# Optimization experiments

Measured on AMD Instinct MI355X. Metric: run time of the kernel, lower is better.

## Reference

```python
import jax, jax.numpy as jnp
import numpy as np

N, E = 50000, 800000          # nodes, edges (before self-loops)
IN, HID, HEADS, OUT = 128, 32, 4, 128
NEG_SLOPE = 0.2               # PyG GATv2Conv default negative_slope


def setup_inputs() -> dict:
    key = jax.random.key(0)
    ks = jax.random.split(key, 16)
    s = 0.05
    f32 = jnp.float32
    return {
        "x": jax.random.normal(ks[0], (N, IN), f32),
        "edge_index": jax.random.randint(ks[1], (2, E), 0, N, jnp.int32),
        # layer 1: in=128 -> heads=4, out=32 (concat)
        "W1l": jax.random.normal(ks[2], (IN, HEADS * HID), f32) * s,
        "b1l": jnp.zeros((HEADS * HID,), f32),
        "W1r": jax.random.normal(ks[3], (IN, HEADS * HID), f32) * s,
        "b1r": jnp.zeros((HEADS * HID,), f32),
        "att1": jax.random.normal(ks[4], (HEADS, HID), f32) * s,
        "bias1": jnp.zeros((HEADS * HID,), f32),
        # layer 2: in=128 -> heads=1, out=128 (mean/no-concat)
        "W2l": jax.random.normal(ks[5], (HEADS * HID, OUT), f32) * s,
        "b2l": jnp.zeros((OUT,), f32),
        "W2r": jax.random.normal(ks[6], (HEADS * HID, OUT), f32) * s,
        "b2r": jnp.zeros((OUT,), f32),
        "att2": jax.random.normal(ks[7], (1, OUT), f32) * s,
        "bias2": jnp.zeros((OUT,), f32),
    }


def _gatv2_conv(x, src, dst, Wl, bl, Wr, br, att, bias, concat):
    """PyG GATv2Conv (share_weights=False), self-loops already in (src, dst)."""
    n = x.shape[0]
    heads, c = att.shape
    xl = (x @ Wl + bl).reshape(n, heads, c)   # source-side transform
    xr = (x @ Wr + br).reshape(n, heads, c)   # target-side transform
    h = jax.nn.leaky_relu(xl[src] + xr[dst], NEG_SLOPE)      # [E, H, C]
    logits = jnp.einsum('ehc,hc->eh', h, att)                # [E, H]
    # segment softmax over incoming edges of each dst node (self-loops make every segment nonempty)
    m = jax.ops.segment_max(logits, dst, num_segments=n)     # [N, H]
    p = jnp.exp(logits - m[dst])
    denom = jax.ops.segment_sum(p, dst, num_segments=n)
    alpha = p / denom[dst]                                   # [E, H]
    out = jax.ops.segment_sum(xl[src] * alpha[:, :, None], dst, num_segments=n)  # [N, H, C]
    out = out.reshape(n, heads * c) if concat else out.mean(axis=1)
    return out + bias


def reference(x, edge_index, W1l, b1l, W1r, b1r, att1, bias1,
              W2l, b2l, W2r, b2r, att2, bias2):
    n = x.shape[0]
    loops = jnp.arange(n, dtype=edge_index.dtype)            # add_self_loops=True
    src = jnp.concatenate([edge_index[0], loops])
    dst = jnp.concatenate([edge_index[1], loops])
    h = jax.nn.elu(_gatv2_conv(x, src, dst, W1l, b1l, W1r, b1r, att1, bias1, True))
    # dropout is identity in eval mode
    return _gatv2_conv(h, src, dst, W2l, b2l, W2r, b2r, att2, bias2, False)
```

## Files before the change

kernel.cpp:

```cpp
#include <hip/hip_runtime.h>
#include <hip/hip_bf16.h>
#include <cstdint>


typedef __attribute__((ext_vector_type(8))) short  bf16x8;
typedef __attribute__((ext_vector_type(4))) float  f32x4;

__device__ inline uint16_t f2bf(float x) {
    union { __hip_bfloat16 b; uint16_t u; } cv;
    cv.b = __float2bfloat16(x);
    return cv.u;
}

__global__ __launch_bounds__(256) void f32_to_bf16(const float* __restrict__ in,
                                                   uint16_t* __restrict__ outp, int n4)
{
    int i = blockIdx.x * blockDim.x + threadIdx.x;
    if (i < n4) {
        float4 v = reinterpret_cast<const float4*>(in)[i];
        ushort4 o = { f2bf(v.x), f2bf(v.y), f2bf(v.z), f2bf(v.w) };
        reinterpret_cast<ushort4*>(outp)[i] = o;
    }
}

__global__ __launch_bounds__(256) void w_to_bf16T(const float* __restrict__ W,
                                                  uint16_t* __restrict__ WT)
{
    int i = blockIdx.x * blockDim.x + threadIdx.x;
    if (i < 128 * 128) {
        int k = i >> 7, c = i & 127;
        WT[c * 128 + k] = f2bf(W[i]);
    }
}

template <bool OUT_BF16>
__global__ __launch_bounds__(256) void gemm_mfma(
    const uint16_t* __restrict__ A, const uint16_t* __restrict__ WT,
    const float* __restrict__ bias, void* __restrict__ Y, int M)
{
    __shared__ uint16_t WT_lds[64][136];
    const int col0 = blockIdx.y * 64;
    const int row0 = blockIdx.x * 128;
    const int tid  = threadIdx.x;
    const int w    = tid >> 6, l = tid & 63;
    const int cl   = l & 15;
    const int kb   = (l >> 4) * 8;

    for (int i = tid; i < 64 * 16; i += 256) {
        const int c = i >> 4, ch = i & 15;
        const uint4 v = *reinterpret_cast<const uint4*>(&WT[(size_t)(col0 + c) * 128 + ch * 8]);
        *reinterpret_cast<uint4*>(&WT_lds[c][ch * 8]) = v;
    }
    __syncthreads();

    const int mrow = row0 + w * 32 + cl;
    const int rA0 = mrow < M ? mrow : M - 1;
    const int rA1 = (mrow + 16) < M ? (mrow + 16) : M - 1;
    const uint16_t* a0p = A + (size_t)rA0 * 128 + kb;
    const uint16_t* a1p = A + (size_t)rA1 * 128 + kb;

    f32x4 acc[2][4] = {};
#pragma unroll
    for (int ks = 0; ks < 4; ++ks) {
        const bf16x8 a0 = *reinterpret_cast<const bf16x8*>(a0p + ks * 32);
        const bf16x8 a1 = *reinterpret_cast<const bf16x8*>(a1p + ks * 32);
#pragma unroll
        for (int n = 0; n < 4; ++n) {
            const bf16x8 b = *reinterpret_cast<const bf16x8*>(&WT_lds[n * 16 + cl][ks * 32 + kb]);
            acc[0][n] = __builtin_amdgcn_mfma_f32_16x16x32_bf16(a0, b, acc[0][n], 0, 0, 0);
            acc[1][n] = __builtin_amdgcn_mfma_f32_16x16x32_bf16(a1, b, acc[1][n], 0, 0, 0);
        }
    }

    const int rbase = row0 + w * 32 + (l >> 4) * 4;
#pragma unroll
    for (int m = 0; m < 2; ++m) {
#pragma unroll
        for (int n = 0; n < 4; ++n) {
            const int col = col0 + n * 16 + cl;
            const float bv = bias[col];
#pragma unroll
            for (int j = 0; j < 4; ++j) {
                const int row = rbase + m * 16 + j;
                if (row < M) {
                    const float v = acc[m][n][j] + bv;
                    if constexpr (OUT_BF16)
                        ((uint16_t*)Y)[(size_t)row * 128 + col] = f2bf(v);
                    else
                        ((float*)Y)[(size_t)row * 128 + col] = v;
                }
            }
        }
    }
}

__global__ __launch_bounds__(256) void hist_kernel(const int* __restrict__ dst, int E,
                                                   int* __restrict__ count)
{
    for (int i = blockIdx.x * blockDim.x + threadIdx.x; i < E;
         i += gridDim.x * blockDim.x)
        atomicAdd(&count[dst[i]], 1);
}

__global__ __launch_bounds__(1024) void scan_offsets(const int* __restrict__ count,
                                                     int* __restrict__ offset,
                                                     int* __restrict__ cursor, int N)
{
    __shared__ int wsum[16];
    __shared__ int carry_s;
    const int tid = threadIdx.x;
    const int lane = tid & 63, w = tid >> 6;
    if (tid == 0) carry_s = 0;
    __syncthreads();
    for (int base = 0; base < N; base += 1024) {
        int i = base + tid;
        int v = (i < N) ? (count[i] + 1) : 0;
        int x = v;
#pragma unroll
        for (int off = 1; off < 64; off <<= 1) {
            int y = __shfl_up(x, off);
            if (lane >= off) x += y;
        }
        if (lane == 63) wsum[w] = x;
        __syncthreads();
        if (tid < 16) {
            int s2 = wsum[tid];
#pragma unroll
            for (int off = 1; off < 16; off <<= 1) {
                int y = __shfl_up(s2, off);
                if (tid >= off) s2 += y;
            }
            wsum[tid] = s2;
        }
        __syncthreads();
        int carry = carry_s;
        int inc = x + ((w > 0) ? wsum[w - 1] : 0) + carry;
        if (i < N) { offset[i] = inc - v; cursor[i] = inc - v; }
        __syncthreads();
        if (tid == 1023) carry_s = inc;
        __syncthreads();
    }
    if (tid == 0) offset[N] = carry_s;
}

__global__ __launch_bounds__(256) void scatter_kernel(const int* __restrict__ src,
                                                      const int* __restrict__ dst, int E,
                                                      int* __restrict__ cursor,
                                                      int* __restrict__ srcids)
{
    for (int i = blockIdx.x * blockDim.x + threadIdx.x; i < E;
         i += gridDim.x * blockDim.x) {
        int p = atomicAdd(&cursor[dst[i]], 1);
        srcids[p] = src[i];
    }
}

__global__ __launch_bounds__(256) void selfloop_kernel(int* __restrict__ cursor,
                                                       int* __restrict__ srcids, int N)
{
    int i = blockIdx.x * blockDim.x + threadIdx.x;
    if (i < N) {
        int p = atomicAdd(&cursor[i], 1);
        srcids[p] = i;
    }
}

template <int HEADS, bool ELU, bool OUT_BF16>
__global__ __launch_bounds__(256) void gat_aggregate(
    const uint32_t* __restrict__ xl2,
    const float* __restrict__ xr,
    const int* __restrict__ offset, const int* __restrict__ srcids,
    const float* __restrict__ att, const float* __restrict__ bias,
    void* __restrict__ out, int N)
{
    const int wid  = (blockIdx.x * blockDim.x + threadIdx.x) >> 6;
    const int lane = threadIdx.x & 63;
    if (wid >= N) return;

    const int f0 = lane * 2;
    const float2 rr = *reinterpret_cast<const float2*>(&xr[(size_t)wid * 128 + f0]);
    const float av0 = att[f0], av1 = att[f0 + 1];

    float acc0 = 0.0f, acc1 = 0.0f, d = 0.0f;
    const int beg = offset[wid], end = offset[wid + 1];

    int i = beg;
    for (; i + 2 <= end; i += 2) {
        const int sA = srcids[i];
        const int sB = srcids[i + 1];
        const uint32_t vA = xl2[(size_t)sA * 64 + lane];
        const uint32_t vB = xl2[(size_t)sB * 64 + lane];
        const float aA0 = __uint_as_float(vA << 16);
        const float aA1 = __uint_as_float(vA & 0xFFFF0000u);
        const float aB0 = __uint_as_float(vB << 16);
        const float aB1 = __uint_as_float(vB & 0xFFFF0000u);
        float tA0 = aA0 + rr.x, tA1 = aA1 + rr.y;
        float tB0 = aB0 + rr.x, tB1 = aB1 + rr.y;
        tA0 = tA0 > 0.0f ? tA0 : 0.2f * tA0;
        tA1 = tA1 > 0.0f ? tA1 : 0.2f * tA1;
        tB0 = tB0 > 0.0f ? tB0 : 0.2f * tB0;
        tB1 = tB1 > 0.0f ? tB1 : 0.2f * tB1;
        float wA = tA0 * av0 + tA1 * av1;
        float wB = tB0 * av0 + tB1 * av1;
        if (HEADS == 4) {
#pragma unroll
            for (int off = 1; off < 16; off <<= 1) {
                wA += __shfl_xor(wA, off);
                wB += __shfl_xor(wB, off);
            }
        } else {
#pragma unroll
            for (int off = 1; off < 64; off <<= 1) {
                wA += __shfl_xor(wA, off);
                wB += __shfl_xor(wB, off);
            }
        }
        const float pA = __expf(wA);
        const float pB = __expf(wB);
        acc0 += aA0 * pA; acc1 += aA1 * pA; d += pA;
        acc0 += aB0 * pB; acc1 += aB1 * pB; d += pB;
    }
    if (i < end) {
        const int s = srcids[i];
        const uint32_t v = xl2[(size_t)s * 64 + lane];
        const float a0 = __uint_as_float(v << 16);
        const float a1 = __uint_as_float(v & 0xFFFF0000u);
        float t0 = a0 + rr.x, t1 = a1 + rr.y;
        t0 = t0 > 0.0f ? t0 : 0.2f * t0;
        t1 = t1 > 0.0f ? t1 : 0.2f * t1;
        float w = t0 * av0 + t1 * av1;
        if (HEADS == 4) {
#pragma unroll
            for (int off = 1; off < 16; off <<= 1) w += __shfl_xor(w, off);
        } else {
#pragma unroll
            for (int off = 1; off < 64; off <<= 1) w += __shfl_xor(w, off);
        }
        const float p = __expf(w);
        acc0 += a0 * p; acc1 += a1 * p; d += p;
    }

    float v0 = acc0 / d + bias[f0];
    float v1 = acc1 / d + bias[f0 + 1];
    if (ELU) {
        v0 = v0 > 0.0f ? v0 : expm1f(v0);
        v1 = v1 > 0.0f ? v1 : expm1f(v1);
    }
    if constexpr (OUT_BF16) {
        const uint32_t pk = (uint32_t)f2bf(v0) | ((uint32_t)f2bf(v1) << 16);
        ((uint32_t*)out)[(size_t)wid * 64 + lane] = pk;
    } else {
        float2 o = { v0, v1 };
        *reinterpret_cast<float2*>(&((float*)out)[(size_t)wid * 128 + f0]) = o;
    }
}

extern "C" void kernel_launch(void* const* d_in, const int* in_sizes, int n_in,
                              void* d_out, int out_size, void* d_ws, size_t ws_size,
                              hipStream_t stream)
{
    const float* x     = (const float*)d_in[0];
    const int*   ei    = (const int*)  d_in[1];
    const float* W1l   = (const float*)d_in[2];
    const float* b1l   = (const float*)d_in[3];
    const float* W1r   = (const float*)d_in[4];
    const float* b1r   = (const float*)d_in[5];
    const float* att1  = (const float*)d_in[6];
    const float* bias1 = (const float*)d_in[7];
    const float* W2l   = (const float*)d_in[8];
    const float* b2l   = (const float*)d_in[9];
    const float* W2r   = (const float*)d_in[10];
    const float* b2r   = (const float*)d_in[11];
    const float* att2  = (const float*)d_in[12];
    const float* bias2 = (const float*)d_in[13];
    float* out = (float*)d_out;

    const int N    = in_sizes[0] / 128;
    const int E    = in_sizes[1] / 2;
    const int Etot = E + N;
    const int* srcp = ei;
    const int* dstp = ei + E;

    int* count  = (int*)d_ws;
    int* offset = count + N;
    int* cursor = offset + N + 1;
    int* srcids = cursor + N;
    size_t int_elems = (size_t)3 * N + 1 + Etot;
    int_elems = (int_elems + 3) & ~(size_t)3;
    uint32_t* base32 = (uint32_t*)d_ws + int_elems;
    uint16_t* x_bf   = (uint16_t*)base32;
    uint16_t* wt1l   = x_bf + (size_t)N * 128;
    uint16_t* wt1r   = wt1l + 128 * 128;
    uint16_t* wt2l   = wt1r + 128 * 128;
    uint16_t* wt2r   = wt2l + 128 * 128;
    float*    xr     = (float*)(wt2r + 128 * 128);
    uint16_t* h_bf   = (uint16_t*)(xr + (size_t)N * 128);
    uint16_t* xl_bf  = h_bf + (size_t)N * 128;
    uint32_t* h2  = (uint32_t*)h_bf;
    uint32_t* xl2 = (uint32_t*)xl_bf;

    f32_to_bf16<<<(N * 32 + 255) / 256, 256, 0, stream>>>(x, x_bf, N * 32);
    w_to_bf16T<<<64, 256, 0, stream>>>(W1l, wt1l);
    w_to_bf16T<<<64, 256, 0, stream>>>(W1r, wt1r);
    w_to_bf16T<<<64, 256, 0, stream>>>(W2l, wt2l);
    w_to_bf16T<<<64, 256, 0, stream>>>(W2r, wt2r);

    hipMemsetAsync(count, 0, (size_t)N * sizeof(int), stream);
    hist_kernel<<<2048, 256, 0, stream>>>(dstp, E, count);
    scan_offsets<<<1, 1024, 0, stream>>>(count, offset, cursor, N);
    scatter_kernel<<<2048, 256, 0, stream>>>(srcp, dstp, E, cursor, srcids);
    selfloop_kernel<<<(N + 255) / 256, 256, 0, stream>>>(cursor, srcids, N);

    dim3 gG((N + 127) / 128, 2);
    const int ablocks = (N + 3) / 4;

    gemm_mfma<true ><<<gG, 256, 0, stream>>>(x_bf, wt1l, b1l, xl_bf, N);
    gemm_mfma<false><<<gG, 256, 0, stream>>>(x_bf, wt1r, b1r, xr,    N);
    gat_aggregate<4, true, true><<<ablocks, 256, 0, stream>>>(
        xl2, xr, offset, srcids, att1, bias1, h_bf, N);
    gemm_mfma<true ><<<gG, 256, 0, stream>>>(h_bf, wt2l, b2l, xl_bf, N);
    gemm_mfma<false><<<gG, 256, 0, stream>>>(h_bf, wt2r, b2r, xr,    N);
    gat_aggregate<1, false, false><<<ablocks, 256, 0, stream>>>(
        xl2, xr, offset, srcids, att2, bias2, out, N);
}
```

Before: 448.2 us.

## Parallelize offset scan, merge weight and self-loop kernels, unroll aggregation by four

Replaces the single-block serial scan over all nodes with a three-kernel multi-block scan (block sums, 64-entry mid scan, apply). It also merges the four weight transpose launches into one and folds the self-loop insertion into the scatter kernel. The edge loop in the aggregation kernel now processes four neighbours per iteration to put more gathers in flight. These changes target the latency of the serial scan and launch overhead, at the cost of extra registers in the aggregation and an assumption that the number of scan blocks is at most 64.

Result: faster. 384.0 us (-14.3%).

```diff
diff --git a/kernel.cpp b/kernel.cpp
--- a/kernel.cpp
+++ b/kernel.cpp
@@ -23,14 +23,18 @@
     }
 }
 
-__global__ __launch_bounds__(256) void w_to_bf16T(const float* __restrict__ W,
-                                                  uint16_t* __restrict__ WT)
+__global__ __launch_bounds__(256) void w4_to_bf16T(
+    const float* __restrict__ W0, const float* __restrict__ W1,
+    const float* __restrict__ W2, const float* __restrict__ W3,
+    uint16_t* __restrict__ T0, uint16_t* __restrict__ T1,
+    uint16_t* __restrict__ T2, uint16_t* __restrict__ T3)
 {
     int i = blockIdx.x * blockDim.x + threadIdx.x;
-    if (i < 128 * 128) {
-        int k = i >> 7, c = i & 127;
-        WT[c * 128 + k] = f2bf(W[i]);
-    }
+    const int which = i >> 14, j = i & 16383;
+    const int k = j >> 7, c = j & 127;
+    const float* W = which == 0 ? W0 : which == 1 ? W1 : which == 2 ? W2 : W3;
+    uint16_t*   T = which == 0 ? T0 : which == 1 ? T1 : which == 2 ? T2 : T3;
+    T[c * 128 + k] = f2bf(W[j]);
 }
 
 template <bool OUT_BF16>
@@ -102,66 +106,94 @@
         atomicAdd(&count[dst[i]], 1);
 }
 
-__global__ __launch_bounds__(1024) void scan_offsets(const int* __restrict__ count,
-                                                     int* __restrict__ offset,
-                                                     int* __restrict__ cursor, int N)
-{
-    __shared__ int wsum[16];
-    __shared__ int carry_s;
+__global__ __launch_bounds__(256) void scan_blocksums(const int* __restrict__ count,
+                                                      int* __restrict__ bsum, int N)
+{
+    __shared__ int wsum[4];
+    const int tid = threadIdx.x, lane = tid & 63, w = tid >> 6;
+    const int base = blockIdx.x * 1024 + tid * 4;
+    int s = 0;
+#pragma unroll
+    for (int j = 0; j < 4; ++j) {
+        int idx = base + j;
+        s += (idx < N) ? (count[idx] + 1) : 0;
+    }
+#pragma unroll
+    for (int off = 1; off < 64; off <<= 1) s += __shfl_xor(s, off);
+    if (lane == 0) wsum[w] = s;
+    __syncthreads();
+    if (tid == 0) bsum[blockIdx.x] = wsum[0] + wsum[1] + wsum[2] + wsum[3];
+}
+
+__global__ __launch_bounds__(64) void scan_mid(const int* __restrict__ bsum,
+                                               int* __restrict__ bpre,
+                                               int* __restrict__ offset, int nb, int N)
+{
     const int tid = threadIdx.x;
-    const int lane = tid & 63, w = tid >> 6;
-    if (tid == 0) carry_s = 0;
+    int v = (tid < nb) ? bsum[tid] : 0;
+    int x = v;
+#pragma unroll
+    for (int off = 1; off < 64; off <<= 1) {
+        int y = __shfl_up(x, off);
+        if (tid >= off) x += y;
+    }
+    if (tid < nb) bpre[tid] = x - v;
+    const int total = __shfl(x, 63);
+    if (tid == 0) offset[N] = total;
+}
+
+__global__ __launch_bounds__(256) void scan_apply(const int* __restrict__ count,
+                                                  const int* __restrict__ bpre,
+                                                  int* __restrict__ offset,
+                                                  int* __restrict__ cursor, int N)
+{
+    __shared__ int wsum[4];
+    const int tid = threadIdx.x, lane = tid & 63, w = tid >> 6;
+    const int base = blockIdx.x * 1024 + tid * 4;
+    int v[4];
+    int s = 0;
+#pragma unroll
+    for (int j = 0; j < 4; ++j) {
+        int idx = base + j;
+        v[j] = (idx < N) ? (count[idx] + 1) : 0;
+        s += v[j];
+    }
+    int x = s;
+#pragma unroll
+    for (int off = 1; off < 64; off <<= 1) {
+        int y = __shfl_up(x, off);
+        if (lane >= off) x += y;
+    }
+    if (lane == 63) wsum[w] = x;
     __syncthreads();
-    for (int base = 0; base < N; base += 1024) {
-        int i = base + tid;
-        int v = (i < N) ? (count[i] + 1) : 0;
-        int x = v;
-#pragma unroll
-        for (int off = 1; off < 64; off <<= 1) {
-            int y = __shfl_up(x, off);
-            if (lane >= off) x += y;
-        }
-        if (lane == 63) wsum[w] = x;
-        __syncthreads();
-        if (tid < 16) {
-            int s2 = wsum[tid];
-#pragma unroll
-            for (int off = 1; off < 16; off <<= 1) {
-                int y = __shfl_up(s2, off);
-                if (tid >= off) s2 += y;
-            }
-            wsum[tid] = s2;
-        }
-        __syncthreads();
-        int carry = carry_s;
-        int inc = x + ((w > 0) ? wsum[w - 1] : 0) + carry;
-        if (i < N) { offset[i] = inc - v; cursor[i] = inc - v; }
-        __syncthreads();
-        if (tid == 1023) carry_s = inc;
-        __syncthreads();
-    }
-    if (tid == 0) offset[N] = carry_s;
+    int wpre = 0;
+#pragma unroll
+    for (int k = 0; k < 4; ++k) wpre += (k < w) ? wsum[k] : 0;
+    int run = bpre[blockIdx.x] + wpre + (x - s);
+#pragma unroll
+    for (int j = 0; j < 4; ++j) {
+        int idx = base + j;
+        if (idx < N) { offset[idx] = run; cursor[idx] = run; }
+        run += v[j];
+    }
 }
 
 __global__ __launch_bounds__(256) void scatter_kernel(const int* __restrict__ src,
-                                                      const int* __restrict__ dst, int E,
+                                                      const int* __restrict__ dst,
+                                                      int E, int Etot,
                                                       int* __restrict__ cursor,
                                                       int* __restrict__ srcids)
 {
-    for (int i = blockIdx.x * blockDim.x + threadIdx.x; i < E;
+    for (int i = blockIdx.x * blockDim.x + threadIdx.x; i < Etot;
          i += gridDim.x * blockDim.x) {
-        int p = atomicAdd(&cursor[dst[i]], 1);
-        srcids[p] = src[i];
-    }
-}
-
-__global__ __launch_bounds__(256) void selfloop_kernel(int* __restrict__ cursor,
-                                                       int* __restrict__ srcids, int N)
-{
-    int i = blockIdx.x * blockDim.x + threadIdx.x;
-    if (i < N) {
-        int p = atomicAdd(&cursor[i], 1);
-        srcids[p] = i;
+        if (i < E) {
+            int p = atomicAdd(&cursor[dst[i]], 1);
+            srcids[p] = src[i];
+        } else {
+            int n = i - E;
+            int p = atomicAdd(&cursor[n], 1);
+            srcids[p] = n;
+        }
     }
 }
 
@@ -180,47 +212,40 @@
     const int f0 = lane * 2;
     const float2 rr = *reinterpret_cast<const float2*>(&xr[(size_t)wid * 128 + f0]);
     const float av0 = att[f0], av1 = att[f0 + 1];
+    constexpr int LIM = (HEADS == 4) ? 16 : 64;
 
     float acc0 = 0.0f, acc1 = 0.0f, d = 0.0f;
     const int beg = offset[wid], end = offset[wid + 1];
 
     int i = beg;
-    for (; i + 2 <= end; i += 2) {
-        const int sA = srcids[i];
-        const int sB = srcids[i + 1];
-        const uint32_t vA = xl2[(size_t)sA * 64 + lane];
-        const uint32_t vB = xl2[(size_t)sB * 64 + lane];
-        const float aA0 = __uint_as_float(vA << 16);
-        const float aA1 = __uint_as_float(vA & 0xFFFF0000u);
-        const float aB0 = __uint_as_float(vB << 16);
-        const float aB1 = __uint_as_float(vB & 0xFFFF0000u);
-        float tA0 = aA0 + rr.x, tA1 = aA1 + rr.y;
-        float tB0 = aB0 + rr.x, tB1 = aB1 + rr.y;
-        tA0 = tA0 > 0.0f ? tA0 : 0.2f * tA0;
-        tA1 = tA1 > 0.0f ? tA1 : 0.2f * tA1;
-        tB0 = tB0 > 0.0f ? tB0 : 0.2f * tB0;
-        tB1 = tB1 > 0.0f ? tB1 : 0.2f * tB1;
-        float wA = tA0 * av0 + tA1 * av1;
-        float wB = tB0 * av0 + tB1 * av1;
-        if (HEADS == 4) {
-#pragma unroll
-            for (int off = 1; off < 16; off <<= 1) {
-                wA += __shfl_xor(wA, off);
-                wB += __shfl_xor(wB, off);
-            }
-        } else {
-#pragma unroll
-            for (int off = 1; off < 64; off <<= 1) {
-                wA += __shfl_xor(wA, off);
-                wB += __shfl_xor(wB, off);
-            }
-        }
-        const float pA = __expf(wA);
-        const float pB = __expf(wB);
-        acc0 += aA0 * pA; acc1 += aA1 * pA; d += pA;
-        acc0 += aB0 * pB; acc1 += aB1 * pB; d += pB;
-    }
-    if (i < end) {
+    for (; i + 4 <= end; i += 4) {
+        int s[4]; uint32_t v[4];
+#pragma unroll
+        for (int c = 0; c < 4; ++c) s[c] = srcids[i + c];
+#pragma unroll
+        for (int c = 0; c < 4; ++c) v[c] = xl2[(size_t)s[c] * 64 + lane];
+        float a0[4], a1[4], wv[4];
+#pragma unroll
+        for (int c = 0; c < 4; ++c) {
+            a0[c] = __uint_as_float(v[c] << 16);
+            a1[c] = __uint_as_float(v[c] & 0xFFFF0000u);
+            float t0 = a0[c] + rr.x, t1 = a1[c] + rr.y;
+            t0 = t0 > 0.0f ? t0 : 0.2f * t0;
+            t1 = t1 > 0.0f ? t1 : 0.2f * t1;
+            wv[c] = t0 * av0 + t1 * av1;
+        }
+#pragma unroll
+        for (int off = 1; off < LIM; off <<= 1) {
+#pragma unroll
+            for (int c = 0; c < 4; ++c) wv[c] += __shfl_xor(wv[c], off);
+        }
+#pragma unroll
+        for (int c = 0; c < 4; ++c) {
+            const float p = __expf(wv[c]);
+            acc0 += a0[c] * p; acc1 += a1[c] * p; d += p;
+        }
+    }
+    for (; i < end; ++i) {
         const int s = srcids[i];
         const uint32_t v = xl2[(size_t)s * 64 + lane];
         const float a0 = __uint_as_float(v << 16);
@@ -229,13 +254,8 @@
         t0 = t0 > 0.0f ? t0 : 0.2f * t0;
         t1 = t1 > 0.0f ? t1 : 0.2f * t1;
         float w = t0 * av0 + t1 * av1;
-        if (HEADS == 4) {
-#pragma unroll
-            for (int off = 1; off < 16; off <<= 1) w += __shfl_xor(w, off);
-        } else {
-#pragma unroll
-            for (int off = 1; off < 64; off <<= 1) w += __shfl_xor(w, off);
-        }
+#pragma unroll
+        for (int off = 1; off < LIM; off <<= 1) w += __shfl_xor(w, off);
         const float p = __expf(w);
         acc0 += a0 * p; acc1 += a1 * p; d += p;
     }
@@ -280,12 +300,15 @@
     const int Etot = E + N;
     const int* srcp = ei;
     const int* dstp = ei + E;
+    const int nb = (N + 1023) / 1024;
 
     int* count  = (int*)d_ws;
     int* offset = count + N;
     int* cursor = offset + N + 1;
-    int* srcids = cursor + N;
-    size_t int_elems = (size_t)3 * N + 1 + Etot;
+    int* bsum   = cursor + N;
+    int* bpre   = bsum + 64;
+    int* srcids = bpre + 64;
+    size_t int_elems = (size_t)3 * N + 129 + Etot;
     int_elems = (int_elems + 3) & ~(size_t)3;
     uint32_t* base32 = (uint32_t*)d_ws + int_elems;
     uint16_t* x_bf   = (uint16_t*)base32;
@@ -296,20 +319,18 @@
     float*    xr     = (float*)(wt2r + 128 * 128);
     uint16_t* h_bf   = (uint16_t*)(xr + (size_t)N * 128);
     uint16_t* xl_bf  = h_bf + (size_t)N * 128;
-    uint32_t* h2  = (uint32_t*)h_bf;
     uint32_t* xl2 = (uint32_t*)xl_bf;
 
     f32_to_bf16<<<(N * 32 + 255) / 256, 256, 0, stream>>>(x, x_bf, N * 32);
-    w_to_bf16T<<<64, 256, 0, stream>>>(W1l, wt1l);
-    w_to_bf16T<<<64, 256, 0, stream>>>(W1r, wt1r);
-    w_to_bf16T<<<64, 256, 0, stream>>>(W2l, wt2l);
-    w_to_bf16T<<<64, 256, 0, stream>>>(W2r, wt2r);
+    w4_to_bf16T<<<256, 256, 0, stream>>>(W1l, W1r, W2l, W2r,
+                                         wt1l, wt1r, wt2l, wt2r);
 
     hipMemsetAsync(count, 0, (size_t)N * sizeof(int), stream);
     hist_kernel<<<2048, 256, 0, stream>>>(dstp, E, count);
-    scan_offsets<<<1, 1024, 0, stream>>>(count, offset, cursor, N);
-    scatter_kernel<<<2048, 256, 0, stream>>>(srcp, dstp, E, cursor, srcids);
-    selfloop_kernel<<<(N + 255) / 256, 256, 0, stream>>>(cursor, srcids, N);
+    scan_blocksums<<<nb, 256, 0, stream>>>(count, bsum, N);
+    scan_mid<<<1, 64, 0, stream>>>(bsum, bpre, offset, nb, N);
+    scan_apply<<<nb, 256, 0, stream>>>(count, bpre, offset, cursor, N);
+    scatter_kernel<<<2048, 256, 0, stream>>>(srcp, dstp, E, Etot, cursor, srcids);
 
     dim3 gG((N + 127) / 128, 2);
     const int ablocks = (N + 3) / 4;
```
